# Kernel tuning notes

Measured on AMD Instinct MI355X. Metric: run time of the kernel, lower is better.

## Reference

```python
import jax, jax.numpy as jnp
import numpy as np

B, N, H = 4, 4096, 1024
NH, HD, M = 16, 64, 256
EPS = 1e-5


def gaussian_orthogonal(m, d, rng):
    # scaling=0: rows are orthogonal blocks scaled by norms of fresh gaussian rows
    blocks = []
    n_blocks = (m + d - 1) // d
    for _ in range(n_blocks):
        q, _ = np.linalg.qr(rng.standard_normal((d, d)))
        blocks.append(q.T)
    mat = np.concatenate(blocks, 0)[:m]
    multiplier = np.linalg.norm(rng.standard_normal((m, d)), axis=1)
    return (multiplier[:, None] * mat).astype(np.float32)


def setup_inputs():
    key = jax.random.key(0)
    keys = iter(jax.random.split(key, 24))
    rng = np.random.default_rng(0)

    def w(din, dout):
        return jax.random.normal(next(keys), (din, dout), jnp.float32) * 0.02

    inp = {
        'x': jax.random.normal(next(keys), (B, N, H), jnp.float32),
        'enc_outputs': jax.random.normal(next(keys), (B, N, H), jnp.float32),
    }
    for p in ('sa', 'ca'):
        for q in ('wq', 'wk', 'wv', 'wo'):
            inp[f'{p}_{q}'] = w(H, H)
            inp[f'{p}_b{q[1]}'] = jnp.zeros((H,), jnp.float32)
        inp[f'{p}_proj'] = jnp.asarray(gaussian_orthogonal(M, HD, rng))
    inp['ff_w1'] = w(H, 4 * H); inp['ff_b1'] = jnp.zeros((4 * H,), jnp.float32)
    inp['ff_w2'] = w(4 * H, H); inp['ff_b2'] = jnp.zeros((H,), jnp.float32)
    for i in (1, 2, 3):
        inp[f'ln{i}_g'] = jnp.ones((H,), jnp.float32)
        inp[f'ln{i}_b'] = jnp.zeros((H,), jnp.float32)
    return inp


def _split(t):
    b, n, _ = t.shape
    return t.reshape(b, n, NH, HD).transpose(0, 2, 1, 3)  # [b,h,n,d]


def _feat(data, proj):
    # FAVOR+ nonnegative softmax kernel features
    dn = HD ** -0.25
    dd = jnp.einsum('bhnd,md->bhnm', data * dn, proj)
    diag = 0.5 * (dn ** 2) * jnp.sum(data * data, -1)  # [b,h,n]
    dd = dd - diag[..., None] - jnp.max(dd, axis=-1, keepdims=True)
    return (M ** -0.5) * (jnp.exp(dd) + 1e-4)


def _attn(q, k, v, wq, bq, wk, bk, wv, bv, wo, bo, proj):
    b, n, _ = q.shape
    Q = _split(q @ wq + bq)
    K = _split(k @ wk + bk)
    V = _split(v @ wv + bv)
    Qp = _feat(Q, proj)  # [b,h,n,m]
    Kp = _feat(K, proj)
    denom = jnp.einsum('bhnm,bhm->bhn', Qp, Kp.sum(2))[..., None]
    ctx = jnp.einsum('bhnm,bhnd->bhmd', Kp, V)          # O(N) linear attention
    out = jnp.einsum('bhnm,bhmd->bhnd', Qp, ctx) / denom
    # faithful to torch .view(B,-1,hidden) WITHOUT head transpose-back
    out = out.reshape(b, -1, H)
    return out @ wo + bo


def _ln(x, g, b):
    mu = jnp.mean(x, -1, keepdims=True)
    var = jnp.mean((x - mu) ** 2, -1, keepdims=True)
    return (x - mu) / jnp.sqrt(var + EPS) * g + b


def reference(x, enc_outputs, sa_wq, sa_bq, sa_wk, sa_bk, sa_wv, sa_bv, sa_wo, sa_bo,
              sa_proj, ca_wq, ca_bq, ca_wk, ca_bk, ca_wv, ca_bv, ca_wo, ca_bo, ca_proj,
              ff_w1, ff_b1, ff_w2, ff_b2, ln1_g, ln1_b, ln2_g, ln2_b, ln3_g, ln3_b):
    h = _ln(x + _attn(x, x, x, sa_wq, sa_bq, sa_wk, sa_bk, sa_wv, sa_bv, sa_wo, sa_bo, sa_proj), ln1_g, ln1_b)
    h = _ln(h + _attn(h, enc_outputs, enc_outputs, ca_wq, ca_bq, ca_wk, ca_bk, ca_wv, ca_bv, ca_wo, ca_bo, ca_proj), ln2_g, ln2_b)
    ff = jax.nn.gelu(h @ ff_w1 + ff_b1, approximate=True) @ ff_w2 + ff_b2  # dropout prob 0 -> identity
    return _ln(h + ff, ln3_g, ln3_b)
```

## Files before the change

### kernel.cpp

```cpp
#include <hip/hip_runtime.h>
#include <hip/hip_bf16.h>

#define B_ 4
#define N_ 4096
#define H_ 1024
#define NH_ 16
#define HD_ 64
#define M_ 256

typedef __attribute__((ext_vector_type(8))) __bf16 bf16x8;
typedef __attribute__((ext_vector_type(4))) float f32x4;
typedef __attribute__((ext_vector_type(4))) unsigned int u32x4;

__device__ __forceinline__ float bf2f(unsigned short u) {
  union { unsigned int i; float f; } x; x.i = ((unsigned int)u) << 16; return x.f;
}
__device__ __forceinline__ unsigned short f2b(float f) {
  __hip_bfloat16 h = __float2bfloat16(f);
  return *(unsigned short*)&h;
}
__device__ __forceinline__ float gelu_f(float x) {
  const float c = 0.7978845608028654f;
  float t = tanhf(c * (x + 0.044715f * x * x * x));
  return 0.5f * x * (1.0f + t);
}

typedef __attribute__((address_space(3))) unsigned int as3_uint;
typedef const __attribute__((address_space(1))) unsigned int as1_uint;
__device__ __forceinline__ void gload16(const void* g, void* l) {
  __builtin_amdgcn_global_load_lds((as1_uint*)g, (as3_uint*)l, 16, 0, 0);
}

template<int ACT>
__launch_bounds__(256)
__global__ void gemm_mfma(const unsigned short* __restrict__ A, int lda,
                          const unsigned short* __restrict__ BT,
                          const float* __restrict__ bias,
                          unsigned short* __restrict__ C, int ldc, int K) {
  __shared__ __align__(16) char LDS[65536];

  const int tid = threadIdx.x;
  const int nwg = gridDim.x * gridDim.y;
  const int lin = blockIdx.y * gridDim.x + blockIdx.x;
  const int mm = (lin & 7) * (nwg >> 3) + (lin >> 3);
  const int bx = mm % gridDim.x, by = mm / gridDim.x;
  const int row0 = by * 128;
  const int col0 = bx * 128;

  const int w = tid >> 6, lane = tid & 63;
  const int wm = w >> 1, wn = w & 1;
  const int ln = lane & 15, hi = lane >> 4;
  const int rswz = (ln & 7) << 4;

  const int srow = w * 8 + (lane >> 3);
  const int schunk = ((lane & 7) ^ (lane >> 3)) * 8;
  const unsigned short* Ag = A + (long long)(row0 + srow) * lda + schunk;
  const unsigned short* Bg = BT + (long long)(col0 + srow) * K + schunk;
  const int ldsw = w * 1024;

  f32x4 acc[4][4];
#pragma unroll
  for (int i = 0; i < 4; ++i)
#pragma unroll
    for (int j = 0; j < 4; ++j) acc[i][j] = (f32x4){0.f, 0.f, 0.f, 0.f};

  auto STAGE = [&](int p, int k0) {
    char* dst = LDS + p * 32768 + ldsw;
#pragma unroll
    for (int i = 0; i < 4; ++i) {
      gload16(Ag + (long long)i * 32 * lda + k0, dst + i * 4096);
      gload16(Bg + (long long)i * 32 * K + k0, dst + 16384 + i * 4096);
    }
  };
  auto COMPUTE = [&](int p) {
    char* AsB = LDS + p * 32768;
    char* BsB = AsB + 16384;
#pragma unroll
    for (int kc = 0; kc < 2; ++kc) {
      const int koff = (kc * 64 + hi * 16) ^ rswz;
      bf16x8 av[4], bv[4];
#pragma unroll
      for (int i = 0; i < 4; ++i)
        av[i] = *(bf16x8*)(AsB + (wm * 64 + i * 16 + ln) * 128 + koff);
#pragma unroll
      for (int j = 0; j < 4; ++j)
        bv[j] = *(bf16x8*)(BsB + (wn * 64 + j * 16 + ln) * 128 + koff);
      __builtin_amdgcn_s_setprio(1);
#pragma unroll
      for (int i = 0; i < 4; ++i)
#pragma unroll
        for (int j = 0; j < 4; ++j)
          acc[i][j] = __builtin_amdgcn_mfma_f32_16x16x32_bf16(av[i], bv[j], acc[i][j], 0, 0, 0);
      __builtin_amdgcn_s_setprio(0);
    }
  };

  STAGE(0, 0);
  __syncthreads();
  int cur = 0;
  for (int k0 = 64; k0 < K; k0 += 64) {
    STAGE(cur ^ 1, k0);
    COMPUTE(cur);
    __syncthreads();
    cur ^= 1;
  }
  COMPUTE(cur);
  __syncthreads();

  char* SB = LDS;
#pragma unroll
  for (int j = 0; j < 4; ++j) {
    const int lcol = wn * 64 + j * 16 + ln;
    const float bj = bias ? bias[col0 + lcol] : 0.0f;
#pragma unroll
    for (int i = 0; i < 4; ++i) {
      const int rb_ = wm * 64 + i * 16 + hi * 4;
#pragma unroll
      for (int r = 0; r < 4; ++r) {
        float v = acc[i][j][r] + bj;
        if (ACT == 1) v = gelu_f(v);
        const int row = rb_ + r;
        *(unsigned short*)(SB + ((row * 256 + lcol * 2) ^ ((row & 7) << 4))) = f2b(v);
      }
    }
  }
  __syncthreads();
#pragma unroll
  for (int p = 0; p < 8; ++p) {
    const int idx = p * 256 + tid;
    const int row = idx >> 4, seg = idx & 15;
    u32x4 v = *(u32x4*)(SB + ((row * 256 + seg * 16) ^ ((row & 7) << 4)));
    __builtin_nontemporal_store(v, (u32x4*)(C + (long long)(row0 + row) * ldc + col0 + seg * 8));
  }
}

__launch_bounds__(256)
__global__ void ctxksum_mfma(const unsigned short* __restrict__ QKV,
                             const unsigned short* __restrict__ pjB,
                             float* __restrict__ ksumP,
                             float* __restrict__ ctxP) {
  __shared__ char Kt[8192];
  __shared__ char Vt[8192];
  __shared__ char Pt[32768];
  __shared__ float rmaxL[4][64];
  __shared__ float ssqL[64];
  const int z = blockIdx.z, b = z >> 4, hh = z & 15;
  const int sp = blockIdx.x;
  const long long n0 = sp * 512;
  const unsigned short* Kg = QKV + (long long)(b * 4096) * 3072 + 1024 + hh * 64;
  const unsigned short* Vg = QKV + (long long)(b * 4096) * 3072 + 2048 + hh * 64;
  const int tid = threadIdx.x;
  const int w = tid >> 6, lane = tid & 63;
  const int ln = lane & 15, hi = lane >> 4;
  const int rswz = (ln & 7) << 4;

  f32x4 accC[4][4];
#pragma unroll
  for (int i = 0; i < 4; ++i)
#pragma unroll
    for (int j = 0; j < 4; ++j) accC[i][j] = (f32x4){0.f, 0.f, 0.f, 0.f};
  float cs[4] = {0.f, 0.f, 0.f, 0.f};

  for (int t = 0; t < 8; ++t) {
    const long long nt = n0 + t * 64;
    __syncthreads();
#pragma unroll
    for (int p = 0; p < 2; ++p) {
      int id = p * 256 + tid;
      int r = id >> 3, c = id & 7;
      gload16(Kg + (nt + r) * 3072 + ((c ^ (r & 7)) * 8), Kt + id * 16);
    }
    {
      int n = tid >> 2, d0 = (tid & 3) * 16;
      const unsigned short* src = Vg + (nt + n) * 3072 + d0;
      ushort4 v0 = *(const ushort4*)src;
      ushort4 v1 = *(const ushort4*)(src + 4);
      ushort4 v2 = *(const ushort4*)(src + 8);
      ushort4 v3 = *(const ushort4*)(src + 12);
      unsigned short vals[16] = {v0.x, v0.y, v0.z, v0.w, v1.x, v1.y, v1.z, v1.w,
                                 v2.x, v2.y, v2.z, v2.w, v3.x, v3.y, v3.z, v3.w};
#pragma unroll
      for (int e = 0; e < 16; ++e) {
        int d = d0 + e;
        *(unsigned short*)(Vt + ((d * 128 + n * 2) ^ ((d & 7) << 4))) = vals[e];
      }
    }
    __syncthreads();

    f32x4 accF[4][4];
#pragma unroll
    for (int i = 0; i < 4; ++i)
#pragma unroll
      for (int j = 0; j < 4; ++j) accF[i][j] = (f32x4){0.f, 0.f, 0.f, 0.f};
#pragma unroll
    for (int kc = 0; kc < 2; ++kc) {
      const int koff = (kc * 64 + hi * 16) ^ rswz;
      bf16x8 av[4], bq[4];
#pragma unroll
      for (int i = 0; i < 4; ++i)
        av[i] = *(bf16x8*)(Kt + (i * 16 + ln) * 128 + koff);
#pragma unroll
      for (int j = 0; j < 4; ++j)
        bq[j] = *(const bf16x8*)(pjB + (w * 64 + j * 16 + ln) * 64 + kc * 32 + hi * 8);
      __builtin_amdgcn_s_setprio(1);
#pragma unroll
      for (int i = 0; i < 4; ++i)
#pragma unroll
        for (int j = 0; j < 4; ++j)
          accF[i][j] = __builtin_amdgcn_mfma_f32_16x16x32_bf16(av[i], bq[j], accF[i][j], 0, 0, 0);
      __builtin_amdgcn_s_setprio(0);
    }

#pragma unroll
    for (int i = 0; i < 4; ++i)
#pragma unroll
      for (int r = 0; r < 4; ++r) {
        float m = fmaxf(fmaxf(accF[i][0][r], accF[i][1][r]), fmaxf(accF[i][2][r], accF[i][3][r]));
        m = fmaxf(m, __shfl_xor(m, 1, 64));
        m = fmaxf(m, __shfl_xor(m, 2, 64));
        m = fmaxf(m, __shfl_xor(m, 4, 64));
        m = fmaxf(m, __shfl_xor(m, 8, 64));
        if (ln == 0) rmaxL[w][i * 16 + hi * 4 + r] = m;
      }
    {
      int r = tid >> 2, q = tid & 3;
      int b0 = (r * 128 + q * 32) ^ ((r & 7) << 4);
      int b1 = (r * 128 + q * 32 + 16) ^ ((r & 7) << 4);
      u32x4 x0 = *(u32x4*)(Kt + b0);
      u32x4 x1 = *(u32x4*)(Kt + b1);
      float s = 0.f;
#pragma unroll
      for (int e = 0; e < 4; ++e) {
        float a0 = bf2f((unsigned short)(x0[e] & 0xffff)), a1 = bf2f((unsigned short)(x0[e] >> 16));
        float a2 = bf2f((unsigned short)(x1[e] & 0xffff)), a3 = bf2f((unsigned short)(x1[e] >> 16));
        s += a0 * a0 + a1 * a1 + a2 * a2 + a3 * a3;
      }
      s += __shfl_xor(s, 1, 64);
      s += __shfl_xor(s, 2, 64);
      if (q == 0) ssqL[r] = s;
    }
    __syncthreads();

    float base[4][4];
#pragma unroll
    for (int i = 0; i < 4; ++i)
#pragma unroll
      for (int r = 0; r < 4; ++r) {
        int row = i * 16 + hi * 4 + r;
        base[i][r] = 0.0625f * ssqL[row] +
                     fmaxf(fmaxf(rmaxL[0][row], rmaxL[1][row]), fmaxf(rmaxL[2][row], rmaxL[3][row]));
      }
#pragma unroll
    for (int i = 0; i < 4; ++i)
#pragma unroll
      for (int j = 0; j < 4; ++j) {
        float v0 = 0.0625f * (expf(accF[i][j][0] - base[i][0]) + 1e-4f);
        float v1 = 0.0625f * (expf(accF[i][j][1] - base[i][1]) + 1e-4f);
        float v2 = 0.0625f * (expf(accF[i][j][2] - base[i][2]) + 1e-4f);
        float v3 = 0.0625f * (expf(accF[i][j][3] - base[i][3]) + 1e-4f);
        cs[j] += v0 + v1 + v2 + v3;
        ushort4 pk;
        pk.x = f2b(v0); pk.y = f2b(v1); pk.z = f2b(v2); pk.w = f2b(v3);
        int m = w * 64 + j * 16 + ln;
        *(ushort4*)(Pt + ((m * 128 + i * 32 + hi * 8) ^ ((m & 7) << 4))) = pk;
      }
    __syncthreads();

#pragma unroll
    for (int kc = 0; kc < 2; ++kc) {
      const int koff = (kc * 64 + hi * 16) ^ rswz;
      bf16x8 am[4], bv[4];
#pragma unroll
      for (int i = 0; i < 4; ++i)
        am[i] = *(bf16x8*)(Pt + (w * 64 + i * 16 + ln) * 128 + koff);
#pragma unroll
      for (int j = 0; j < 4; ++j)
        bv[j] = *(bf16x8*)(Vt + (j * 16 + ln) * 128 + koff);
      __builtin_amdgcn_s_setprio(1);
#pragma unroll
      for (int i = 0; i < 4; ++i)
#pragma unroll
        for (int j = 0; j < 4; ++j)
          accC[i][j] = __builtin_amdgcn_mfma_f32_16x16x32_bf16(am[i], bv[j], accC[i][j], 0, 0, 0);
      __builtin_amdgcn_s_setprio(0);
    }
  }

#pragma unroll
  for (int j = 0; j < 4; ++j) {
    cs[j] += __shfl_xor(cs[j], 16, 64);
    cs[j] += __shfl_xor(cs[j], 32, 64);
  }
  if (hi == 0) {
#pragma unroll
    for (int j = 0; j < 4; ++j)
      ksumP[((long long)z * 8 + sp) * 256 + w * 64 + j * 16 + ln] = cs[j];
  }

  float* ctxPs = ctxP + ((long long)z * 8 + sp) * 16384;
#pragma unroll
  for (int dh = 0; dh < 2; ++dh) {
    __syncthreads();
#pragma unroll
    for (int i = 0; i < 4; ++i)
#pragma unroll
      for (int jj = 0; jj < 2; ++jj) {
        int j = dh * 2 + jj;
#pragma unroll
        for (int r = 0; r < 4; ++r) {
          int m = w * 64 + i * 16 + hi * 4 + r;
          int dl = jj * 16 + ln;
          *(float*)(Pt + ((m * 128 + dl * 4) ^ ((m & 7) << 4))) = accC[i][j][r];
        }
      }
    __syncthreads();
#pragma unroll
    for (int p = 0; p < 8; ++p) {
      int idx = p * 256 + tid;
      int row = idx >> 3, seg = idx & 7;
      u32x4 v = *(u32x4*)(Pt + ((row * 128 + seg * 16) ^ ((row & 7) << 4)));
      __builtin_nontemporal_store(v, (u32x4*)(ctxPs + dh * 8192 + row * 32 + seg * 4));
    }
  }
}

__launch_bounds__(256)
__global__ void ctx_fin(const float* __restrict__ ctxP, const float* __restrict__ ksumP,
                        unsigned short* __restrict__ ctxbf, float* __restrict__ ksumF) {
  __shared__ float acc[16384];
  const int z = blockIdx.x;
  const int tid = threadIdx.x;
  const float* base = ctxP + (long long)z * 8 * 16384;
  for (int i = tid; i < 16384; i += 256) {
    float s = 0.f;
#pragma unroll
    for (int q = 0; q < 8; ++q) s += base[(long long)q * 16384 + i];
    acc[i] = s;
  }
  {
    const float* kb = ksumP + (long long)z * 8 * 256;
    float s = 0.f;
#pragma unroll
    for (int q = 0; q < 8; ++q) s += kb[q * 256 + tid];
    ksumF[z * 256 + tid] = s;
  }
  __syncthreads();
  unsigned short* dst = ctxbf + (long long)z * 16384;
  for (int cc = tid; cc < 2048; cc += 256) {
    int mh = cc >> 10, rem = cc & 1023, d = rem >> 4, cl = rem & 15;
    int m0 = mh * 128 + cl * 8;
    int dh = d >> 5, dl = d & 31;
    ushort4 o0, o1;
    o0.x = f2b(acc[dh * 8192 + (m0 + 0) * 32 + dl]);
    o0.y = f2b(acc[dh * 8192 + (m0 + 1) * 32 + dl]);
    o0.z = f2b(acc[dh * 8192 + (m0 + 2) * 32 + dl]);
    o0.w = f2b(acc[dh * 8192 + (m0 + 3) * 32 + dl]);
    o1.x = f2b(acc[dh * 8192 + (m0 + 4) * 32 + dl]);
    o1.y = f2b(acc[dh * 8192 + (m0 + 5) * 32 + dl]);
    o1.z = f2b(acc[dh * 8192 + (m0 + 6) * 32 + dl]);
    o1.w = f2b(acc[dh * 8192 + (m0 + 7) * 32 + dl]);
    unsigned short* p = dst + (long long)mh * 8192 + (d * 16 + (cl ^ (d & 7))) * 8;
    *(ushort4*)p = o0;
    *(ushort4*)(p + 4) = o1;
  }
}

__launch_bounds__(256)
__global__ void ao_fused(const unsigned short* __restrict__ QKV,
                         const unsigned short* __restrict__ pjB,
                         const float* __restrict__ ksum,
                         const unsigned short* __restrict__ ctxbf,
                         unsigned short* __restrict__ AO) {
  __shared__ char Qt[8192];
  __shared__ char Ps[32768];
  __shared__ char Ch[32768];
  __shared__ float rmaxL[4][64];
  __shared__ float ssqL[64];
  __shared__ float dprt[4][64];
  __shared__ float denomS[64];
  const int z = blockIdx.z, b = z >> 4, hh = z & 15;
  const int n0 = blockIdx.x * 64;
  const unsigned short* Qg = QKV + (long long)(b * 4096) * 3072 + hh * 64;
  const int tid = threadIdx.x;
  const int w = tid >> 6, lane = tid & 63;
  const int ln = lane & 15, hi = lane >> 4;
  const int rswz = (ln & 7) << 4;

#pragma unroll
  for (int p = 0; p < 8; ++p) {
    int id = p * 256 + tid;
    gload16(ctxbf + (long long)z * 16384 + id * 8, Ch + id * 16);
  }
#pragma unroll
  for (int p = 0; p < 2; ++p) {
    int id = p * 256 + tid;
    int r = id >> 3, c = id & 7;
    gload16(Qg + (long long)(n0 + r) * 3072 + ((c ^ (r & 7)) * 8), Qt + id * 16);
  }
  __syncthreads();

  f32x4 accF[4][4];
#pragma unroll
  for (int i = 0; i < 4; ++i)
#pragma unroll
    for (int j = 0; j < 4; ++j) accF[i][j] = (f32x4){0.f, 0.f, 0.f, 0.f};
#pragma unroll
  for (int kc = 0; kc < 2; ++kc) {
    const int koff = (kc * 64 + hi * 16) ^ rswz;
    bf16x8 av[4], bq[4];
#pragma unroll
    for (int i = 0; i < 4; ++i)
      av[i] = *(bf16x8*)(Qt + (i * 16 + ln) * 128 + koff);
#pragma unroll
    for (int j = 0; j < 4; ++j)
      bq[j] = *(const bf16x8*)(pjB + (w * 64 + j * 16 + ln) * 64 + kc * 32 + hi * 8);
    __builtin_amdgcn_s_setprio(1);
#pragma unroll
    for (int i = 0; i < 4; ++i)
#pragma unroll
      for (int j = 0; j < 4; ++j)
        accF[i][j] = __builtin_amdgcn_mfma_f32_16x16x32_bf16(av[i], bq[j], accF[i][j], 0, 0, 0);
    __builtin_amdgcn_s_setprio(0);
  }

#pragma unroll
  for (int i = 0; i < 4; ++i)
#pragma unroll
    for (int r = 0; r < 4; ++r) {
      float m = fmaxf(fmaxf(accF[i][0][r], accF[i][1][r]), fmaxf(accF[i][2][r], accF[i][3][r]));
      m = fmaxf(m, __shfl_xor(m, 1, 64));
      m = fmaxf(m, __shfl_xor(m, 2, 64));
      m = fmaxf(m, __shfl_xor(m, 4, 64));
      m = fmaxf(m, __shfl_xor(m, 8, 64));
      if (ln == 0) rmaxL[w][i * 16 + hi * 4 + r] = m;
    }
  {
    int r = tid >> 2, q = tid & 3;
    int b0 = (r * 128 + q * 32) ^ ((r & 7) << 4);
    int b1 = (r * 128 + q * 32 + 16) ^ ((r & 7) << 4);
    u32x4 x0 = *(u32x4*)(Qt + b0);
    u32x4 x1 = *(u32x4*)(Qt + b1);
    float s = 0.f;
#pragma unroll
    for (int e = 0; e < 4; ++e) {
      float a0 = bf2f((unsigned short)(x0[e] & 0xffff)), a1 = bf2f((unsigned short)(x0[e] >> 16));
      float a2 = bf2f((unsigned short)(x1[e] & 0xffff)), a3 = bf2f((unsigned short)(x1[e] >> 16));
      s += a0 * a0 + a1 * a1 + a2 * a2 + a3 * a3;
    }
    s += __shfl_xor(s, 1, 64);
    s += __shfl_xor(s, 2, 64);
    if (q == 0) ssqL[r] = s;
  }
  __syncthreads();

  float ks[4];
#pragma unroll
  for (int j = 0; j < 4; ++j) ks[j] = ksum[z * 256 + w * 64 + j * 16 + ln];
#pragma unroll
  for (int i = 0; i < 4; ++i)
#pragma unroll
    for (int r = 0; r < 4; ++r) {
      int n = i * 16 + hi * 4 + r;
      float base = 0.0625f * ssqL[n] +
                   fmaxf(fmaxf(rmaxL[0][n], rmaxL[1][n]), fmaxf(rmaxL[2][n], rmaxL[3][n]));
      float dp = 0.f;
#pragma unroll
      for (int j = 0; j < 4; ++j) {
        float v = 0.0625f * (expf(accF[i][j][r] - base) + 1e-4f);
        unsigned short vb = f2b(v);
        int m = w * 64 + j * 16 + ln;
        *(unsigned short*)(Ps + n * 512 + ((m * 2) ^ ((n & 7) << 4))) = vb;
        dp += bf2f(vb) * ks[j];
      }
      dp += __shfl_xor(dp, 1, 64);
      dp += __shfl_xor(dp, 2, 64);
      dp += __shfl_xor(dp, 4, 64);
      dp += __shfl_xor(dp, 8, 64);
      if (ln == 0) dprt[w][n] = dp;
    }
  __syncthreads();
  if (tid < 64) denomS[tid] = dprt[0][tid] + dprt[1][tid] + dprt[2][tid] + dprt[3][tid];

  f32x4 accO[4];
#pragma unroll
  for (int j = 0; j < 4; ++j) accO[j] = (f32x4){0.f, 0.f, 0.f, 0.f};
#pragma unroll
  for (int mh = 0; mh < 2; ++mh) {
#pragma unroll
    for (int ms = 0; ms < 4; ++ms) {
      const int koff = (ms * 64 + hi * 16);
      bf16x8 ap = *(bf16x8*)(Ps + (w * 16 + ln) * 512 + ((mh * 256 + koff) ^ rswz));
      bf16x8 bc[4];
#pragma unroll
      for (int j = 0; j < 4; ++j)
        bc[j] = *(bf16x8*)(Ch + mh * 16384 + (j * 16 + ln) * 256 + (koff ^ rswz));
      __builtin_amdgcn_s_setprio(1);
#pragma unroll
      for (int j = 0; j < 4; ++j)
        accO[j] = __builtin_amdgcn_mfma_f32_16x16x32_bf16(ap, bc[j], accO[j], 0, 0, 0);
      __builtin_amdgcn_s_setprio(0);
    }
  }
  __syncthreads();

  float inv[4];
#pragma unroll
  for (int r = 0; r < 4; ++r) inv[r] = 1.0f / denomS[w * 16 + hi * 4 + r];
  char* Ct = Qt;
#pragma unroll
  for (int j = 0; j < 4; ++j)
#pragma unroll
    for (int r = 0; r < 4; ++r) {
      int n = w * 16 + hi * 4 + r;
      int d = j * 16 + ln;
      *(unsigned short*)(Ct + ((n * 128 + d * 2) ^ ((n & 7) << 4))) = f2b(accO[j][r] * inv[r]);
    }
  __syncthreads();
#pragma unroll
  for (int p = 0; p < 2; ++p) {
    int idx = p * 256 + tid;
    int row = idx >> 3, seg = idx & 7;
    u32x4 v = *(u32x4*)(Ct + ((row * 128 + seg * 16) ^ ((row & 7) << 4)));
    *(u32x4*)(AO + (long long)(b * 4096 + n0 + row) * 1024 + hh * 64 + seg * 8) = v;
  }
}

__launch_bounds__(256)
__global__ void wt_cvt(const float* __restrict__ in, unsigned short* __restrict__ out,
                       int K, int N) {
  __shared__ float t[32][33];
  int k0 = blockIdx.y * 32, n0 = blockIdx.x * 32;
  int tx = threadIdx.x & 31, ty = threadIdx.x >> 5;
  for (int r = ty; r < 32; r += 8) t[r][tx] = in[(long long)(k0 + r) * N + n0 + tx];
  __syncthreads();
  for (int r = ty; r < 32; r += 8) out[(long long)(n0 + r) * K + k0 + tx] = f2b(t[tx][r]);
}

__launch_bounds__(256)
__global__ void projB_cvt(const float* __restrict__ proj, unsigned short* __restrict__ out) {
  int i = blockIdx.x * 256 + threadIdx.x;
  out[i] = f2b(0.35355339059327373f * proj[i]);
}

__launch_bounds__(256)
__global__ void bias_cat(const float* __restrict__ b0, const float* __restrict__ b1,
                         const float* __restrict__ b2, float* __restrict__ out) {
  int i = blockIdx.x * 256 + threadIdx.x;
  float v;
  if (i < 1024) v = b0[i];
  else if (i < 2048) v = b1[i - 1024];
  else v = b2[i - 2048];
  out[i] = v;
}

__launch_bounds__(256)
__global__ void cvt_bf16(const float* __restrict__ in, unsigned short* __restrict__ out,
                         long long n) {
  long long stride = (long long)gridDim.x * 1024;
  for (long long i = ((long long)blockIdx.x * 256 + threadIdx.x) * 4; i < n; i += stride) {
    float4 v = *(const float4*)&in[i];
    ushort4 o;
    o.x = f2b(v.x); o.y = f2b(v.y); o.z = f2b(v.z); o.w = f2b(v.w);
    *(ushort4*)&out[i] = o;
  }
}

__launch_bounds__(256)
__global__ void ln_k(const float* __restrict__ resf, const unsigned short* __restrict__ resb,
                     const unsigned short* __restrict__ po,
                     const float* __restrict__ g, const float* __restrict__ be,
                     float* __restrict__ outf, unsigned short* __restrict__ outb) {
  long long row = blockIdx.x;
  int t = threadIdx.x;
  float x0, x1, x2, x3;
  if (resf) {
    float4 va = ((const float4*)(resf + row * H_))[t];
    x0 = va.x; x1 = va.y; x2 = va.z; x3 = va.w;
  } else {
    ushort4 va = ((const ushort4*)(resb + row * H_))[t];
    x0 = bf2f(va.x); x1 = bf2f(va.y); x2 = bf2f(va.z); x3 = bf2f(va.w);
  }
  {
    ushort4 vp = ((const ushort4*)(po + row * H_))[t];
    x0 += bf2f(vp.x); x1 += bf2f(vp.y); x2 += bf2f(vp.z); x3 += bf2f(vp.w);
  }
  float s = x0 + x1 + x2 + x3;
  float q = x0 * x0 + x1 * x1 + x2 * x2 + x3 * x3;
#pragma unroll
  for (int m = 1; m < 64; m <<= 1) { s += __shfl_xor(s, m, 64); q += __shfl_xor(q, m, 64); }
  __shared__ float ssum[4], ssq[4];
  int w = t >> 6, lane = t & 63;
  if (lane == 0) { ssum[w] = s; ssq[w] = q; }
  __syncthreads();
  s = ssum[0] + ssum[1] + ssum[2] + ssum[3];
  q = ssq[0] + ssq[1] + ssq[2] + ssq[3];
  float mean = s * (1.0f / H_);
  float var = q * (1.0f / H_) - mean * mean;
  float rstd = rsqrtf(var + 1e-5f);
  float4 vg = ((const float4*)g)[t];
  float4 vbe = ((const float4*)be)[t];
  float o0 = (x0 - mean) * rstd * vg.x + vbe.x;
  float o1 = (x1 - mean) * rstd * vg.y + vbe.y;
  float o2 = (x2 - mean) * rstd * vg.z + vbe.z;
  float o3 = (x3 - mean) * rstd * vg.w + vbe.w;
  if (outf) {
    float4 o; o.x = o0; o.y = o1; o.z = o2; o.w = o3;
    ((float4*)(outf + row * H_))[t] = o;
  }
  if (outb) {
    ushort4 ob; ob.x = f2b(o0); ob.y = f2b(o1); ob.z = f2b(o2); ob.w = f2b(o3);
    ((ushort4*)(outb + row * H_))[t] = ob;
  }
}

extern "C" void kernel_launch(void* const* d_in, const int* in_sizes, int n_in,
                              void* d_out, int out_size, void* d_ws, size_t ws_size,
                              hipStream_t stream) {
  (void)in_sizes; (void)n_in; (void)out_size; (void)ws_size;
  const float* x      = (const float*)d_in[0];
  const float* enc    = (const float*)d_in[1];
  const float* sa_w[4] = {(const float*)d_in[2], (const float*)d_in[4], (const float*)d_in[6], (const float*)d_in[8]};
  const float* sa_b[4] = {(const float*)d_in[3], (const float*)d_in[5], (const float*)d_in[7], (const float*)d_in[9]};
  const float* sa_pj  = (const float*)d_in[10];
  const float* ca_w[4] = {(const float*)d_in[11], (const float*)d_in[13], (const float*)d_in[15], (const float*)d_in[17]};
  const float* ca_b[4] = {(const float*)d_in[12], (const float*)d_in[14], (const float*)d_in[16], (const float*)d_in[18]};
  const float* ca_pj  = (const float*)d_in[19];
  const float* ff_w1  = (const float*)d_in[20];
  const float* ff_b1  = (const float*)d_in[21];
  const float* ff_w2  = (const float*)d_in[22];
  const float* ff_b2  = (const float*)d_in[23];
  const float* ln1_g  = (const float*)d_in[24];
  const float* ln1_b  = (const float*)d_in[25];
  const float* ln2_g  = (const float*)d_in[26];
  const float* ln2_b  = (const float*)d_in[27];
  const float* ln3_g  = (const float*)d_in[28];
  const float* ln3_b  = (const float*)d_in[29];

  float* ws = (float*)d_ws;
  unsigned short* XB = (unsigned short*)(ws);
  unsigned short* EB = (unsigned short*)(ws + 8388608LL);
  unsigned short* QKVb = (unsigned short*)(ws + 16777216LL);
  unsigned short* PO = (unsigned short*)(ws + 41943040LL);
  float* ctxP = ws + 41943040LL;
  unsigned short* MIDB = PO;
  unsigned short* FO = (unsigned short*)(ws + 50331648LL);
  unsigned short* WTph = (unsigned short*)(ws + 52428800LL);
  unsigned short* pjB = (unsigned short*)(ws + 54525952LL);
  float* ksumP = ws + 54542336LL;
  float* ksumF = ws + 54673408LL;
  unsigned short* ctxbf = (unsigned short*)(ws + 55607296LL);
  float* biasC = ws + 56131584LL;

  unsigned short* ff1T = EB;
  unsigned short* ff2T = EB + 4194304LL;
  unsigned short* pjB_sa = pjB, *pjB_ca = pjB + 16384;

  dim3 blk(256, 1, 1);
  const int LDQ = 3072;

  projB_cvt<<<dim3(64), blk, 0, stream>>>(sa_pj, pjB_sa);
  projB_cvt<<<dim3(64), blk, 0, stream>>>(ca_pj, pjB_ca);
  cvt_bf16<<<dim3(2048), blk, 0, stream>>>(x, XB, 16777216LL);

  auto attn_core = [&](const unsigned short* pj, const float* wo_bias) {
    ctxksum_mfma<<<dim3(8, 1, 64), blk, 0, stream>>>(QKVb, pj, ksumP, ctxP);
    ctx_fin<<<dim3(64), blk, 0, stream>>>(ctxP, ksumP, ctxbf, ksumF);
    ao_fused<<<dim3(64, 1, 64), blk, 0, stream>>>(QKVb, pj, ksumF, ctxbf, EB);
    gemm_mfma<0><<<dim3(8, 128), blk, 0, stream>>>(EB, H_, WTph + 3145728, wo_bias, PO, H_, H_);
  };

  for (int i = 0; i < 4; ++i)
    wt_cvt<<<dim3(32, 32), blk, 0, stream>>>(sa_w[i], WTph + (long long)i * 1048576, H_, H_);
  bias_cat<<<dim3(12), blk, 0, stream>>>(sa_b[0], sa_b[1], sa_b[2], biasC);
  gemm_mfma<0><<<dim3(24, 128), blk, 0, stream>>>(XB, H_, WTph, biasC, QKVb, LDQ, H_);
  attn_core(pjB_sa, sa_b[3]);
  ln_k<<<dim3(16384), blk, 0, stream>>>(x, nullptr, PO, ln1_g, ln1_b, nullptr, XB);

  cvt_bf16<<<dim3(2048), blk, 0, stream>>>(enc, EB, 16777216LL);
  for (int i = 0; i < 4; ++i)
    wt_cvt<<<dim3(32, 32), blk, 0, stream>>>(ca_w[i], WTph + (long long)i * 1048576, H_, H_);
  bias_cat<<<dim3(8), blk, 0, stream>>>(ca_b[1], ca_b[2], nullptr, biasC);
  gemm_mfma<0><<<dim3(8, 128), blk, 0, stream>>>(XB, H_, WTph, ca_b[0], QKVb, LDQ, H_);
  gemm_mfma<0><<<dim3(16, 128), blk, 0, stream>>>(EB, H_, WTph + 1048576, biasC, QKVb + 1024, LDQ, H_);
  attn_core(pjB_ca, ca_b[3]);
  ln_k<<<dim3(16384), blk, 0, stream>>>(nullptr, XB, PO, ln2_g, ln2_b, nullptr, XB);

  wt_cvt<<<dim3(128, 32), blk, 0, stream>>>(ff_w1, ff1T, H_, 4096);
  wt_cvt<<<dim3(32, 128), blk, 0, stream>>>(ff_w2, ff2T, 4096, H_);
  for (int c = 0; c < 4; ++c) {
    const long long co = (long long)c * 4096 * H_;
    gemm_mfma<1><<<dim3(32, 32), blk, 0, stream>>>(XB + co, H_, ff1T, ff_b1, MIDB, 4096, H_);
    gemm_mfma<0><<<dim3(8, 32), blk, 0, stream>>>(MIDB, 4096, ff2T, ff_b2, FO, H_, 4096);
    ln_k<<<dim3(4096), blk, 0, stream>>>(nullptr, XB + co, FO, ln3_g, ln3_b,
                                         (float*)d_out + co, nullptr);
  }
}
```

Measured before the change: 1.493 ms.

## Transpose feature MFMA operands so row reductions use fewer shuffles; ksum via MFMA

Both feature kernels now compute the projection MFMA with operands swapped, producing the transposed tile (features x tokens). Per-token max and denominator reductions then need only two cross-lane shuffles instead of four per row. In the context kernel, the key-feature column sum is produced by an extra MFMA against a ones vector instead of scalar accumulation. The trade-off is scalar 2-byte LDS stores for the feature tiles instead of packed ushort4 stores, extra MFMA work, and ksum now summed from bf16-rounded features.

```diff
diff --git a/kernel.cpp b/kernel.cpp
--- a/kernel.cpp
+++ b/kernel.cpp
@@ -23,6 +23,11 @@
   const float c = 0.7978845608028654f;
   float t = tanhf(c * (x + 0.044715f * x * x * x));
   return 0.5f * x * (1.0f + t);
+}
+__device__ __forceinline__ bf16x8 ones8() {
+  union { unsigned int u[4]; bf16x8 v; } o;
+  o.u[0] = 0x3F803F80u; o.u[1] = 0x3F803F80u; o.u[2] = 0x3F803F80u; o.u[3] = 0x3F803F80u;
+  return o.v;
 }
 
 typedef __attribute__((address_space(3))) unsigned int as3_uint;
@@ -153,13 +158,16 @@
   const int w = tid >> 6, lane = tid & 63;
   const int ln = lane & 15, hi = lane >> 4;
   const int rswz = (ln & 7) << 4;
+  const bf16x8 onesf = ones8();
 
   f32x4 accC[4][4];
 #pragma unroll
   for (int i = 0; i < 4; ++i)
 #pragma unroll
     for (int j = 0; j < 4; ++j) accC[i][j] = (f32x4){0.f, 0.f, 0.f, 0.f};
-  float cs[4] = {0.f, 0.f, 0.f, 0.f};
+  f32x4 accK[4];
+#pragma unroll
+  for (int i = 0; i < 4; ++i) accK[i] = (f32x4){0.f, 0.f, 0.f, 0.f};
 
   for (int t = 0; t < 8; ++t) {
     const long long nt = n0 + t * 64;
@@ -187,41 +195,41 @@
     }
     __syncthreads();
 
-    f32x4 accF[4][4];
+    f32x4 accT[4][4];
 #pragma unroll
     for (int i = 0; i < 4; ++i)
 #pragma unroll
-      for (int j = 0; j < 4; ++j) accF[i][j] = (f32x4){0.f, 0.f, 0.f, 0.f};
+      for (int j = 0; j < 4; ++j) accT[i][j] = (f32x4){0.f, 0.f, 0.f, 0.f};
 #pragma unroll
     for (int kc = 0; kc < 2; ++kc) {
       const int koff = (kc * 64 + hi * 16) ^ rswz;
-      bf16x8 av[4], bq[4];
-#pragma unroll
-      for (int i = 0; i < 4; ++i)
-        av[i] = *(bf16x8*)(Kt + (i * 16 + ln) * 128 + koff);
-#pragma unroll
-      for (int j = 0; j < 4; ++j)
-        bq[j] = *(const bf16x8*)(pjB + (w * 64 + j * 16 + ln) * 64 + kc * 32 + hi * 8);
+      bf16x8 kv[4], bq[4];
+#pragma unroll
+      for (int nj = 0; nj < 4; ++nj)
+        kv[nj] = *(bf16x8*)(Kt + (nj * 16 + ln) * 128 + koff);
+#pragma unroll
+      for (int mi = 0; mi < 4; ++mi)
+        bq[mi] = *(const bf16x8*)(pjB + (w * 64 + mi * 16 + ln) * 64 + kc * 32 + hi * 8);
       __builtin_amdgcn_s_setprio(1);
 #pragma unroll
-      for (int i = 0; i < 4; ++i)
-#pragma unroll
-        for (int j = 0; j < 4; ++j)
-          accF[i][j] = __builtin_amdgcn_mfma_f32_16x16x32_bf16(av[i], bq[j], accF[i][j], 0, 0, 0);
+      for (int mi = 0; mi < 4; ++mi)
+#pragma unroll
+        for (int nj = 0; nj < 4; ++nj)
+          accT[mi][nj] = __builtin_amdgcn_mfma_f32_16x16x32_bf16(bq[mi], kv[nj], accT[mi][nj], 0, 0, 0);
       __builtin_amdgcn_s_setprio(0);
     }
 
 #pragma unroll
-    for (int i = 0; i < 4; ++i)
-#pragma unroll
-      for (int r = 0; r < 4; ++r) {
-        float m = fmaxf(fmaxf(accF[i][0][r], accF[i][1][r]), fmaxf(accF[i][2][r], accF[i][3][r]));
-        m = fmaxf(m, __shfl_xor(m, 1, 64));
-        m = fmaxf(m, __shfl_xor(m, 2, 64));
-        m = fmaxf(m, __shfl_xor(m, 4, 64));
-        m = fmaxf(m, __shfl_xor(m, 8, 64));
-        if (ln == 0) rmaxL[w][i * 16 + hi * 4 + r] = m;
-      }
+    for (int nj = 0; nj < 4; ++nj) {
+      float mx = accT[0][nj][0];
+#pragma unroll
+      for (int mi = 0; mi < 4; ++mi)
+#pragma unroll
+        for (int r = 0; r < 4; ++r) mx = fmaxf(mx, accT[mi][nj][r]);
+      mx = fmaxf(mx, __shfl_xor(mx, 16, 64));
+      mx = fmaxf(mx, __shfl_xor(mx, 32, 64));
+      if (hi == 0) rmaxL[w][nj * 16 + ln] = mx;
+    }
     {
       int r = tid >> 2, q = tid & 3;
       int b0 = (r * 128 + q * 32) ^ ((r & 7) << 4);
@@ -241,29 +249,24 @@
     }
     __syncthreads();
 
-    float base[4][4];
-#pragma unroll
-    for (int i = 0; i < 4; ++i)
-#pragma unroll
-      for (int r = 0; r < 4; ++r) {
-        int row = i * 16 + hi * 4 + r;
-        base[i][r] = 0.0625f * ssqL[row] +
-                     fmaxf(fmaxf(rmaxL[0][row], rmaxL[1][row]), fmaxf(rmaxL[2][row], rmaxL[3][row]));
-      }
-#pragma unroll
-    for (int i = 0; i < 4; ++i)
-#pragma unroll
-      for (int j = 0; j < 4; ++j) {
-        float v0 = 0.0625f * (expf(accF[i][j][0] - base[i][0]) + 1e-4f);
-        float v1 = 0.0625f * (expf(accF[i][j][1] - base[i][1]) + 1e-4f);
-        float v2 = 0.0625f * (expf(accF[i][j][2] - base[i][2]) + 1e-4f);
-        float v3 = 0.0625f * (expf(accF[i][j][3] - base[i][3]) + 1e-4f);
-        cs[j] += v0 + v1 + v2 + v3;
-        ushort4 pk;
-        pk.x = f2b(v0); pk.y = f2b(v1); pk.z = f2b(v2); pk.w = f2b(v3);
-        int m = w * 64 + j * 16 + ln;
-        *(ushort4*)(Pt + ((m * 128 + i * 32 + hi * 8) ^ ((m & 7) << 4))) = pk;
-      }
+    float base[4];
+#pragma unroll
+    for (int nj = 0; nj < 4; ++nj) {
+      int n = nj * 16 + ln;
+      base[nj] = 0.0625f * ssqL[n] +
+                 fmaxf(fmaxf(rmaxL[0][n], rmaxL[1][n]), fmaxf(rmaxL[2][n], rmaxL[3][n]));
+    }
+#pragma unroll
+    for (int mi = 0; mi < 4; ++mi)
+#pragma unroll
+      for (int nj = 0; nj < 4; ++nj)
+#pragma unroll
+        for (int r = 0; r < 4; ++r) {
+          float v = 0.0625f * (expf(accT[mi][nj][r] - base[nj]) + 1e-4f);
+          int m = w * 64 + mi * 16 + hi * 4 + r;
+          int n = nj * 16 + ln;
+          *(unsigned short*)(Pt + ((m * 128 + n * 2) ^ ((m & 7) << 4))) = f2b(v);
+        }
     __syncthreads();
 
 #pragma unroll
@@ -282,19 +285,19 @@
 #pragma unroll
         for (int j = 0; j < 4; ++j)
           accC[i][j] = __builtin_amdgcn_mfma_f32_16x16x32_bf16(am[i], bv[j], accC[i][j], 0, 0, 0);
+#pragma unroll
+      for (int i = 0; i < 4; ++i)
+        accK[i] = __builtin_amdgcn_mfma_f32_16x16x32_bf16(am[i], onesf, accK[i], 0, 0, 0);
       __builtin_amdgcn_s_setprio(0);
     }
   }
 
-#pragma unroll
-  for (int j = 0; j < 4; ++j) {
-    cs[j] += __shfl_xor(cs[j], 16, 64);
-    cs[j] += __shfl_xor(cs[j], 32, 64);
-  }
-  if (hi == 0) {
-#pragma unroll
-    for (int j = 0; j < 4; ++j)
-      ksumP[((long long)z * 8 + sp) * 256 + w * 64 + j * 16 + ln] = cs[j];
+  if (ln == 0) {
+#pragma unroll
+    for (int mi = 0; mi < 4; ++mi)
+#pragma unroll
+      for (int r = 0; r < 4; ++r)
+        ksumP[((long long)z * 8 + sp) * 256 + w * 64 + mi * 16 + hi * 4 + r] = accK[mi][r];
   }
 
   float* ctxPs = ctxP + ((long long)z * 8 + sp) * 16384;
@@ -378,6 +381,7 @@
   __shared__ float ssqL[64];
   __shared__ float dprt[4][64];
   __shared__ float denomS[64];
+  __shared__ float ksL[256];
   const int z = blockIdx.z, b = z >> 4, hh = z & 15;
   const int n0 = blockIdx.x * 64;
   const unsigned short* Qg = QKV + (long long)(b * 4096) * 3072 + hh * 64;
@@ -397,43 +401,44 @@
     int r = id >> 3, c = id & 7;
     gload16(Qg + (long long)(n0 + r) * 3072 + ((c ^ (r & 7)) * 8), Qt + id * 16);
   }
-  __syncthreads();
-
-  f32x4 accF[4][4];
+  ksL[tid] = ksum[z * 256 + tid];
+  __syncthreads();
+
+  f32x4 accT[4][4];
 #pragma unroll
   for (int i = 0; i < 4; ++i)
 #pragma unroll
-    for (int j = 0; j < 4; ++j) accF[i][j] = (f32x4){0.f, 0.f, 0.f, 0.f};
+    for (int j = 0; j < 4; ++j) accT[i][j] = (f32x4){0.f, 0.f, 0.f, 0.f};
 #pragma unroll
   for (int kc = 0; kc < 2; ++kc) {
     const int koff = (kc * 64 + hi * 16) ^ rswz;
-    bf16x8 av[4], bq[4];
-#pragma unroll
-    for (int i = 0; i < 4; ++i)
-      av[i] = *(bf16x8*)(Qt + (i * 16 + ln) * 128 + koff);
-#pragma unroll
-    for (int j = 0; j < 4; ++j)
-      bq[j] = *(const bf16x8*)(pjB + (w * 64 + j * 16 + ln) * 64 + kc * 32 + hi * 8);
+    bf16x8 qv[4], bq[4];
+#pragma unroll
+    for (int nj = 0; nj < 4; ++nj)
+      qv[nj] = *(bf16x8*)(Qt + (nj * 16 + ln) * 128 + koff);
+#pragma unroll
+    for (int mi = 0; mi < 4; ++mi)
+      bq[mi] = *(const bf16x8*)(pjB + (w * 64 + mi * 16 + ln) * 64 + kc * 32 + hi * 8);
     __builtin_amdgcn_s_setprio(1);
 #pragma unroll
-    for (int i = 0; i < 4; ++i)
-#pragma unroll
-      for (int j = 0; j < 4; ++j)
-        accF[i][j] = __builtin_amdgcn_mfma_f32_16x16x32_bf16(av[i], bq[j], accF[i][j], 0, 0, 0);
+    for (int mi = 0; mi < 4; ++mi)
+#pragma unroll
+      for (int nj = 0; nj < 4; ++nj)
+        accT[mi][nj] = __builtin_amdgcn_mfma_f32_16x16x32_bf16(bq[mi], qv[nj], accT[mi][nj], 0, 0, 0);
     __builtin_amdgcn_s_setprio(0);
   }
 
 #pragma unroll
-  for (int i = 0; i < 4; ++i)
-#pragma unroll
-    for (int r = 0; r < 4; ++r) {
-      float m = fmaxf(fmaxf(accF[i][0][r], accF[i][1][r]), fmaxf(accF[i][2][r], accF[i][3][r]));
-      m = fmaxf(m, __shfl_xor(m, 1, 64));
-      m = fmaxf(m, __shfl_xor(m, 2, 64));
-      m = fmaxf(m, __shfl_xor(m, 4, 64));
-      m = fmaxf(m, __shfl_xor(m, 8, 64));
-      if (ln == 0) rmaxL[w][i * 16 + hi * 4 + r] = m;
-    }
+  for (int nj = 0; nj < 4; ++nj) {
+    float mx = accT[0][nj][0];
+#pragma unroll
+    for (int mi = 0; mi < 4; ++mi)
+#pragma unroll
+      for (int r = 0; r < 4; ++r) mx = fmaxf(mx, accT[mi][nj][r]);
+    mx = fmaxf(mx, __shfl_xor(mx, 16, 64));
+    mx = fmaxf(mx, __shfl_xor(mx, 32, 64));
+    if (hi == 0) rmaxL[w][nj * 16 + ln] = mx;
+  }
   {
     int r = tid >> 2, q = tid & 3;
     int b0 = (r * 128 + q * 32) ^ ((r & 7) << 4);
@@ -453,31 +458,39 @@
   }
   __syncthreads();
 
-  float ks[4];
-#pragma unroll
-  for (int j = 0; j < 4; ++j) ks[j] = ksum[z * 256 + w * 64 + j * 16 + ln];
-#pragma unroll
-  for (int i = 0; i < 4; ++i)
-#pragma unroll
-    for (int r = 0; r < 4; ++r) {
-      int n = i * 16 + hi * 4 + r;
-      float base = 0.0625f * ssqL[n] +
-                   fmaxf(fmaxf(rmaxL[0][n], rmaxL[1][n]), fmaxf(rmaxL[2][n], rmaxL[3][n]));
-      float dp = 0.f;
-#pragma unroll
-      for (int j = 0; j < 4; ++j) {
-        float v = 0.0625f * (expf(accF[i][j][r] - base) + 1e-4f);
+  float base[4];
+#pragma unroll
+  for (int nj = 0; nj < 4; ++nj) {
+    int n = nj * 16 + ln;
+    base[nj] = 0.0625f * ssqL[n] +
+               fmaxf(fmaxf(rmaxL[0][n], rmaxL[1][n]), fmaxf(rmaxL[2][n], rmaxL[3][n]));
+  }
+  float ksv[4][4];
+#pragma unroll
+  for (int mi = 0; mi < 4; ++mi)
+#pragma unroll
+    for (int r = 0; r < 4; ++r)
+      ksv[mi][r] = ksL[w * 64 + mi * 16 + hi * 4 + r];
+  float dp[4] = {0.f, 0.f, 0.f, 0.f};
+#pragma unroll
+  for (int mi = 0; mi < 4; ++mi)
+#pragma unroll
+    for (int nj = 0; nj < 4; ++nj)
+#pragma unroll
+      for (int r = 0; r < 4; ++r) {
+        float v = 0.0625f * (expf(accT[mi][nj][r] - base[nj]) + 1e-4f);
         unsigned short vb = f2b(v);
-        int m = w * 64 + j * 16 + ln;
+        int m = w * 64 + mi * 16 + hi * 4 + r;
+        int n = nj * 16 + ln;
         *(unsigned short*)(Ps + n * 512 + ((m * 2) ^ ((n & 7) << 4))) = vb;
-        dp += bf2f(vb) * ks[j];
+        dp[nj] += bf2f(vb) * ksv[mi][r];
       }
-      dp += __shfl_xor(dp, 1, 64);
-      dp += __shfl_xor(dp, 2, 64);
-      dp += __shfl_xor(dp, 4, 64);
-      dp += __shfl_xor(dp, 8, 64);
-      if (ln == 0) dprt[w][n] = dp;
-    }
+#pragma unroll
+  for (int nj = 0; nj < 4; ++nj) {
+    dp[nj] += __shfl_xor(dp[nj], 16, 64);
+    dp[nj] += __shfl_xor(dp[nj], 32, 64);
+    if (hi == 0) dprt[w][nj * 16 + ln] = dp[nj];
+  }
   __syncthreads();
   if (tid < 64) denomS[tid] = dprt[0][tid] + dprt[1][tid] + dprt[2][tid] + dprt[3][tid];
 
```

After: 1.358 ms. 9.1% less time.
